# Kernel optimization log

Measured on AMD Instinct MI355X. Metric: run time of the kernel, lower is better.

Reference implementation:

```python
import jax, jax.numpy as jnp
import numpy as np

B, N = 32768, 20            # batch nodes, temporal neighbors
NF, EF, TF = 172, 172, 100  # node / edge / time feature dims
E = NF + TF                 # query_dim = 272
KD = NF + EF + TF           # key_dim = 444
H = 2                       # heads
HD = E // H                 # head dim 136
OUT = NF                    # output_dimension defaults to n_node_features
NEG = jnp.float32(-1e30)


def setup_inputs() -> dict:
    key = jax.random.key(0)
    ks = jax.random.split(key, 20)
    s = 0.02
    return {
        "src_node_features": jax.random.normal(ks[0], (B, NF), jnp.float32),
        "src_time_features": jax.random.normal(ks[1], (B, 1, TF), jnp.float32),
        "neighbor_features": jax.random.normal(ks[2], (B, N, NF), jnp.float32),
        "neighbor_time_features": jax.random.normal(ks[3], (B, N, TF), jnp.float32),
        "edge_features": jax.random.normal(ks[4], (B, N, EF), jnp.float32),
        "neighbor_mask": jax.random.bernoulli(ks[5], 0.3, (B, N)),
        # nn.MultiheadAttention params (separate q/k/v projections since kdim!=embed_dim)
        "q_w": jax.random.normal(ks[6], (E, E), jnp.float32) * s,
        "k_w": jax.random.normal(ks[7], (E, KD), jnp.float32) * s,
        "v_w": jax.random.normal(ks[8], (E, KD), jnp.float32) * s,
        "q_b": jnp.zeros((E,), jnp.float32),
        "k_b": jnp.zeros((E,), jnp.float32),
        "v_b": jnp.zeros((E,), jnp.float32),
        "out_w": jax.random.normal(ks[9], (E, E), jnp.float32) * s,
        "out_b": jnp.zeros((E,), jnp.float32),
        # merger MLP: Linear(E+NF -> OUT), ReLU, Linear(OUT -> OUT)
        "m1_w": jax.random.normal(ks[10], (OUT, E + NF), jnp.float32) * s,
        "m1_b": jnp.zeros((OUT,), jnp.float32),
        "m2_w": jax.random.normal(ks[11], (OUT, OUT), jnp.float32) * s,
        "m2_b": jnp.zeros((OUT,), jnp.float32),
    }


def reference(src_node_features, src_time_features, neighbor_features,
              neighbor_time_features, edge_features, neighbor_mask,
              q_w, k_w, v_w, q_b, k_b, v_b, out_w, out_b,
              m1_w, m1_b, m2_w, m2_b):
    b = src_node_features.shape[0]
    # single query per node: [B, E]
    query = jnp.concatenate([src_node_features, src_time_features[:, 0, :]], axis=1)
    # keys/values: [B, N, KD]
    kv = jnp.concatenate([neighbor_features, edge_features, neighbor_time_features], axis=2)

    # nodes with no valid neighbor: unmask position 0 (matches torch clone/set trick)
    invalid = jnp.all(neighbor_mask, axis=1)                      # [B]
    mask = neighbor_mask.at[:, 0].set(
        jnp.where(invalid, False, neighbor_mask[:, 0]))

    q = (query @ q_w.T + q_b).reshape(b, H, HD)                   # [B,H,HD]
    k = (kv @ k_w.T + k_b).reshape(b, N, H, HD)                   # [B,N,H,HD]
    v = (kv @ v_w.T + v_b).reshape(b, N, H, HD)

    scores = jnp.einsum('bhd,bnhd->bhn', q, k) / jnp.sqrt(jnp.float32(HD))
    scores = jnp.where(mask[:, None, :], NEG, scores)
    attn = jax.nn.softmax(scores, axis=-1)                        # [B,H,N]
    attn_weights = attn.mean(axis=1)                              # averaged over heads [B,N]

    ctx = jnp.einsum('bhn,bnhd->bhd', attn, v).reshape(b, E)
    attn_out = ctx @ out_w.T + out_b                              # [B,E]
    attn_out = jnp.where(invalid[:, None], 0.0, attn_out)

    merged = jnp.concatenate([attn_out, src_node_features], axis=1)
    hidden = jax.nn.relu(merged @ m1_w.T + m1_b)
    output = hidden @ m2_w.T + m2_b                               # [B,OUT]
    return output, attn_weights
```

## Files before the change

### kernel.cpp

```cpp
#include <hip/hip_runtime.h>
#include <hip/hip_bf16.h>
#include <math.h>

#define NF 172
#define TF_ 100
#define EF 172
#define EDIM 272
#define KD 444
#define NNB 20
#define HD 136
#define OUT_D 172

typedef __attribute__((ext_vector_type(4))) float f32x4;
typedef __attribute__((ext_vector_type(8))) __bf16 bf16x8;
typedef __attribute__((ext_vector_type(4))) __bf16 bf16x4;

__global__ void sniff_k(const unsigned char* __restrict__ m, int* __restrict__ flag) {
    __shared__ int c1, c2;
    if (threadIdx.x == 0) { c1 = 0; c2 = 0; }
    __syncthreads();
    for (int k = 0; k < 4; ++k) {
        int p = threadIdx.x * 4 + k;
        unsigned char v = m[p];
        if ((p & 3) != 0 && v)          atomicOr(&c1, 1);
        if ((p & 3) == 3 && v == 0x3f)  atomicOr(&c2, 1);
    }
    __syncthreads();
    if (threadIdx.x == 0) flag[0] = c2 ? 2 : (c1 ? 1 : 0);
}

#define BKP 40

__global__ __launch_bounds__(256) void gemm_mfma_k(
    const float* __restrict__ A0, int a0_cols, int a0_stride,
    const float* __restrict__ A1, int a1_stride,
    const float* __restrict__ W, int w_stride, int w_nn,
    const float* __restrict__ bias,
    const float* __restrict__ invalf,
    int relu,
    float* __restrict__ C, int c_stride,
    int N, int K)
{
    __shared__ __bf16 As[128][BKP];
    __shared__ __bf16 Bs[128][BKP];

    const int tid  = threadIdx.x;
    const int lane = tid & 63;
    const int wv   = tid >> 6;
    const int wr   = wv >> 1;
    const int wc   = wv & 1;
    const int lr   = lane & 15;
    const int lg   = lane >> 4;
    const int m0   = blockIdx.x * 128;
    const int n0   = blockIdx.y * 128;

    f32x4 acc[4][4];
#pragma unroll
    for (int i = 0; i < 4; ++i)
#pragma unroll
        for (int j = 0; j < 4; ++j) acc[i][j] = (f32x4)(0.f);

    const int srow = tid >> 1;
    const int sch0 = (tid & 1) * 4;
    const int tkk  = tid >> 3;
    const int tcb  = (tid & 7) * 16;

    const int ktiles = (K + 31) / 32;

    for (int t = 0; t < ktiles; ++t) {
        const int k0 = t * 32;

#pragma unroll
        for (int i = 0; i < 4; ++i) {
            const int ch = sch0 + i;
            const int k  = k0 + ch * 4;
            float4 v = make_float4(0.f, 0.f, 0.f, 0.f);
            if (k < K) {
                const float* p = (k < a0_cols)
                    ? (A0 + (size_t)(m0 + srow) * a0_stride + k)
                    : (A1 + (size_t)(m0 + srow) * a1_stride + (k - a0_cols));
                v = *(const float4*)p;
            }
            bf16x4 b;
            b[0] = (__bf16)v.x; b[1] = (__bf16)v.y;
            b[2] = (__bf16)v.z; b[3] = (__bf16)v.w;
            *(bf16x4*)&As[srow][ch * 4] = b;
        }

        if (!w_nn) {
#pragma unroll
            for (int i = 0; i < 4; ++i) {
                const int ch = sch0 + i;
                const int k  = k0 + ch * 4;
                float4 v = make_float4(0.f, 0.f, 0.f, 0.f);
                if (k < K && (n0 + srow) < N)
                    v = *(const float4*)(W + (size_t)(n0 + srow) * w_stride + k);
                bf16x4 b;
                b[0] = (__bf16)v.x; b[1] = (__bf16)v.y;
                b[2] = (__bf16)v.z; b[3] = (__bf16)v.w;
                *(bf16x4*)&Bs[srow][ch * 4] = b;
            }
        } else {
#pragma unroll
            for (int i = 0; i < 4; ++i) {
                const int c = tcb + i * 4;
                float4 v = make_float4(0.f, 0.f, 0.f, 0.f);
                if ((k0 + tkk) < K && (n0 + c + 3) < N)
                    v = *(const float4*)(W + (size_t)(k0 + tkk) * w_stride + n0 + c);
                Bs[c + 0][tkk] = (__bf16)v.x;
                Bs[c + 1][tkk] = (__bf16)v.y;
                Bs[c + 2][tkk] = (__bf16)v.z;
                Bs[c + 3][tkk] = (__bf16)v.w;
            }
        }
        __syncthreads();

        bf16x8 af[4], bfr[4];
#pragma unroll
        for (int f = 0; f < 4; ++f) {
            af[f]  = *(const bf16x8*)&As[wr * 64 + f * 16 + lr][lg * 8];
            bfr[f] = *(const bf16x8*)&Bs[wc * 64 + f * 16 + lr][lg * 8];
        }
#pragma unroll
        for (int fm = 0; fm < 4; ++fm)
#pragma unroll
            for (int fn = 0; fn < 4; ++fn)
                acc[fm][fn] = __builtin_amdgcn_mfma_f32_16x16x32_bf16(
                    af[fm], bfr[fn], acc[fm][fn], 0, 0, 0);
        __syncthreads();
    }

    float bv[4];
#pragma unroll
    for (int fn = 0; fn < 4; ++fn) {
        const int col = n0 + wc * 64 + fn * 16 + lr;
        bv[fn] = (bias && col < N) ? bias[col] : 0.f;
    }
#pragma unroll
    for (int fm = 0; fm < 4; ++fm) {
#pragma unroll
        for (int j = 0; j < 4; ++j) {
            const int row = m0 + wr * 64 + fm * 16 + lg * 4 + j;
            float zf = 1.f;
            if (invalf && invalf[row] != 0.f) zf = 0.f;
#pragma unroll
            for (int fn = 0; fn < 4; ++fn) {
                const int col = n0 + wc * 64 + fn * 16 + lr;
                if (col < N) {
                    float v = acc[fm][fn][j] + bv[fn];
                    if (relu) v = fmaxf(v, 0.f);
                    C[(size_t)row * c_stride + col] = v * zf;
                }
            }
        }
    }
}

__device__ __forceinline__ float dot4(float4 a, float4 b) {
    return a.x * b.x + a.y * b.y + a.z * b.z + a.w * b.w;
}

__global__ __launch_bounds__(256) void attn_flash_k(
    const float* __restrict__ nf, const float* __restrict__ ef,
    const float* __restrict__ ntf,
    const unsigned char* __restrict__ maskp,
    const int* __restrict__ mode_p,
    const float* __restrict__ qk,
    float* __restrict__ wkv,
    float* __restrict__ invalf,
    float* __restrict__ attnw)
{
    const int lane = threadIdx.x & 63;
    const int wv   = threadIdx.x >> 6;
    const int b    = blockIdx.x * 4 + wv;
    const int mode = mode_p[0];

    int mv = 0;
    if (lane < NNB) {
        if (mode == 0)      mv = ((const int*)maskp)[(size_t)b * NNB + lane] != 0;
        else if (mode == 1) mv = maskp[(size_t)b * NNB + lane] != 0;
        else                mv = ((const float*)maskp)[(size_t)b * NNB + lane] != 0.f;
    }
    unsigned long long bal = __ballot(lane < NNB && mv);
    const int inv = ((bal & 0xFFFFFULL) == 0xFFFFFULL);
    if (inv && lane == 0) mv = 0;
    if (lane == 0) invalf[b] = (float)inv;

    const float* qrow = qk + (size_t)b * 888;
    const float4 z4 = make_float4(0.f, 0.f, 0.f, 0.f);
    float4 q0a = *(const float4*)(qrow + lane * 4);
    float4 q1a = *(const float4*)(qrow + KD + lane * 4);
    float4 q0b = z4, q1b = z4;
    if (lane < 47) {
        q0b = *(const float4*)(qrow + (64 + lane) * 4);
        q1b = *(const float4*)(qrow + KD + (64 + lane) * 4);
    }

    const size_t rbase = (size_t)b * NNB;
    const float* pA;
    if (lane < 43) pA = nf + rbase * NF + lane * 4;
    else           pA = ef + rbase * EF + (lane - 43) * 4;
    const float* pB;
    int strideB;
    if (lane < 22) { pB = ef  + rbase * EF  + (21 + lane) * 4; strideB = EF;  }
    else           { pB = ntf + rbase * TF_ + (lane - 22) * 4; strideB = TF_; }

    const float scal = 0.08574929257125441f;
    float4 acc0a = z4, acc0b = z4, acc1a = z4, acc1b = z4;
    float m0 = -3.4e38f, m1 = -3.4e38f, s0 = 0.f, s1 = 0.f;
    float mys0 = 0.f, mys1 = 0.f;

#pragma unroll 5
    for (int n = 0; n < NNB; ++n) {
        float4 kA = *(const float4*)pA;
        pA += NF;
        float4 kB = z4;
        if (lane < 47) {
            kB = *(const float4*)pB;
            pB += strideB;
        }

        float p0 = dot4(q0a, kA) + dot4(q0b, kB);
        float p1 = dot4(q1a, kA) + dot4(q1b, kB);
#pragma unroll
        for (int off = 32; off; off >>= 1) {
            p0 += __shfl_xor(p0, off);
            p1 += __shfl_xor(p1, off);
        }

        const int mn = __shfl(mv, n);
        const float sc0 = mn ? -1e30f : p0 * scal;
        const float sc1 = mn ? -1e30f : p1 * scal;
        if (lane == n) { mys0 = sc0; mys1 = sc1; }

        {
            const float nm = fmaxf(m0, sc0);
            const float f  = expf(m0 - nm);
            const float p  = expf(sc0 - nm);
            s0 = s0 * f + p;
            acc0a.x = acc0a.x * f + p * kA.x;  acc0a.y = acc0a.y * f + p * kA.y;
            acc0a.z = acc0a.z * f + p * kA.z;  acc0a.w = acc0a.w * f + p * kA.w;
            acc0b.x = acc0b.x * f + p * kB.x;  acc0b.y = acc0b.y * f + p * kB.y;
            acc0b.z = acc0b.z * f + p * kB.z;  acc0b.w = acc0b.w * f + p * kB.w;
            m0 = nm;
        }
        {
            const float nm = fmaxf(m1, sc1);
            const float f  = expf(m1 - nm);
            const float p  = expf(sc1 - nm);
            s1 = s1 * f + p;
            acc1a.x = acc1a.x * f + p * kA.x;  acc1a.y = acc1a.y * f + p * kA.y;
            acc1a.z = acc1a.z * f + p * kA.z;  acc1a.w = acc1a.w * f + p * kA.w;
            acc1b.x = acc1b.x * f + p * kB.x;  acc1b.y = acc1b.y * f + p * kB.y;
            acc1b.z = acc1b.z * f + p * kB.z;  acc1b.w = acc1b.w * f + p * kB.w;
            m1 = nm;
        }
    }

    const float r0 = 1.f / s0;
    const float r1 = 1.f / s1;

    if (lane < NNB)
        attnw[(size_t)b * NNB + lane] =
            0.5f * (expf(mys0 - m0) * r0 + expf(mys1 - m1) * r1);

    float* wrow = wkv + (size_t)b * 888;
    float4 o;
    o.x = acc0a.x * r0; o.y = acc0a.y * r0; o.z = acc0a.z * r0; o.w = acc0a.w * r0;
    *(float4*)(wrow + lane * 4) = o;
    o.x = acc1a.x * r1; o.y = acc1a.y * r1; o.z = acc1a.z * r1; o.w = acc1a.w * r1;
    *(float4*)(wrow + KD + lane * 4) = o;
    if (lane < 47) {
        o.x = acc0b.x * r0; o.y = acc0b.y * r0; o.z = acc0b.z * r0; o.w = acc0b.w * r0;
        *(float4*)(wrow + (64 + lane) * 4) = o;
        o.x = acc1b.x * r1; o.y = acc1b.y * r1; o.z = acc1b.z * r1; o.w = acc1b.w * r1;
        *(float4*)(wrow + KD + (64 + lane) * 4) = o;
    }
}

extern "C" void kernel_launch(void* const* d_in, const int* in_sizes, int n_in,
                              void* d_out, int out_size, void* d_ws, size_t ws_size,
                              hipStream_t stream) {
    const float* src_node = (const float*)d_in[0];
    const float* src_time = (const float*)d_in[1];
    const float* nfp      = (const float*)d_in[2];
    const float* ntfp     = (const float*)d_in[3];
    const float* efp      = (const float*)d_in[4];
    const unsigned char* maskp = (const unsigned char*)d_in[5];
    const float* q_w   = (const float*)d_in[6];
    const float* k_w   = (const float*)d_in[7];
    const float* v_w   = (const float*)d_in[8];
    const float* q_b   = (const float*)d_in[9];
    const float* v_b   = (const float*)d_in[11];
    const float* out_w = (const float*)d_in[12];
    const float* out_b = (const float*)d_in[13];
    const float* m1_w  = (const float*)d_in[14];
    const float* m1_b  = (const float*)d_in[15];
    const float* m2_w  = (const float*)d_in[16];
    const float* m2_b  = (const float*)d_in[17];

    const int B = in_sizes[0] / NF;

    float* ws   = (float*)d_ws;
    int*   flag = (int*)d_ws;
    float* Qb   = ws + 16;
    float* qkb  = Qb + (size_t)B * 272;
    float* invb = qkb + (size_t)B * 888;
    float* aob  = qkb;
    float* hidb = Qb;
    float* outp  = (float*)d_out;
    float* attnw = outp + (size_t)B * OUT_D;

    const int gm = B / 128;

    sniff_k<<<1, 256, 0, stream>>>(maskp, flag);

    gemm_mfma_k<<<dim3(gm, 3), 256, 0, stream>>>(
        src_node, NF, NF, src_time, TF_,
        q_w, EDIM, 0, q_b, nullptr, 0, Qb, EDIM, EDIM, EDIM);

    for (int h = 0; h < 2; ++h) {
        gemm_mfma_k<<<dim3(gm, 4), 256, 0, stream>>>(
            Qb + h * HD, HD, EDIM, nullptr, 0,
            k_w + (size_t)h * HD * KD, KD, 1, nullptr, nullptr, 0,
            qkb + h * KD, 888, KD, HD);
    }

    attn_flash_k<<<B / 4, 256, 0, stream>>>(nfp, efp, ntfp, maskp, flag,
                                            qkb, qkb, invb, attnw);

    for (int h = 0; h < 2; ++h) {
        gemm_mfma_k<<<dim3(gm, 2), 256, 0, stream>>>(
            qkb + h * KD, KD, 888, nullptr, 0,
            v_w + (size_t)h * HD * KD, KD, 0, v_b + h * HD, nullptr, 0,
            Qb + h * HD, EDIM, HD, KD);
    }

    gemm_mfma_k<<<dim3(gm, 3), 256, 0, stream>>>(
        Qb, EDIM, EDIM, nullptr, 0,
        out_w, EDIM, 0, out_b, invb, 0, aob, EDIM, EDIM, EDIM);

    gemm_mfma_k<<<dim3(gm, 2), 256, 0, stream>>>(
        aob, EDIM, EDIM, src_node, NF,
        m1_w, KD, 0, m1_b, nullptr, 1, hidb, OUT_D, OUT_D, KD);

    gemm_mfma_k<<<dim3(gm, 2), 256, 0, stream>>>(
        hidb, OUT_D, OUT_D, nullptr, 0,
        m2_w, OUT_D, 0, m2_b, nullptr, 0, outp, OUT_D, OUT_D, OUT_D);
}
```

Measured before the change: 691.7 us.

## Fold Q·K and V·out weights into precomputed matrices, double-buffer GEMM, split attention

A prep kernel precomputes combined weights: q_w^T·k_w per head (GT, with a folded bias) and v_w^T·out_w (MT, with a folded bias). This replaces the Q GEMM, the two per-head QK GEMMs, the two V GEMMs and the out GEMM with one 272→888 GEMM and one 888→272 GEMM. The generic GEMM gains LDS double buffering with register prefetch and drops the transposed-weight path. The attention kernel splits each row's 20 neighbors across two waves, computes the softmax non-online through LDS, and merges partial accumulators. The weight folding is redone on every call, which adds a small prep kernel and enlarges the K dimension of the final GEMM.

```diff
diff --git a/kernel.cpp b/kernel.cpp
--- a/kernel.cpp
+++ b/kernel.cpp
@@ -29,20 +29,73 @@
     if (threadIdx.x == 0) flag[0] = c2 ? 2 : (c1 ? 1 : 0);
 }
 
+__global__ __launch_bounds__(256) void prep_k(
+    const float* __restrict__ q_w, const float* __restrict__ k_w,
+    const float* __restrict__ v_w, const float* __restrict__ q_b,
+    const float* __restrict__ v_b, const float* __restrict__ out_w,
+    const float* __restrict__ out_b,
+    float* __restrict__ GT, float* __restrict__ gb,
+    float* __restrict__ MT, float* __restrict__ mb)
+{
+    const int blk = blockIdx.x;
+    const int tid = threadIdx.x;
+    if (blk < 888) {
+        const int j = blk, h = j / 444, jj = j - h * 444;
+        for (int k = tid; k < 272; k += 256) {
+            float acc = 0.f;
+#pragma unroll 4
+            for (int c = 0; c < 136; ++c)
+                acc += q_w[(size_t)(h * 136 + c) * 272 + k] *
+                       k_w[(size_t)(h * 136 + c) * 444 + jj];
+            GT[(size_t)j * 272 + k] = acc;
+        }
+    } else if (blk < 888 + 272) {
+        const int j = blk - 888;
+        for (int r = tid; r < 888; r += 256) {
+            const int h = r / 444, d = r - h * 444;
+            float acc = 0.f;
+#pragma unroll 4
+            for (int c = 0; c < 136; ++c)
+                acc += v_w[(size_t)(h * 136 + c) * 444 + d] *
+                       out_w[(size_t)j * 272 + h * 136 + c];
+            MT[(size_t)j * 888 + r] = acc;
+        }
+    } else if (blk < 888 + 272 + 4) {
+        const int j = (blk - 888 - 272) * 256 + tid;
+        if (j < 888) {
+            const int h = j / 444, jj = j - h * 444;
+            float acc = 0.f;
+#pragma unroll 4
+            for (int c = 0; c < 136; ++c)
+                acc += q_b[h * 136 + c] * k_w[(size_t)(h * 136 + c) * 444 + jj];
+            gb[j] = acc;
+        }
+    } else {
+        const int j = (blk - 888 - 272 - 4) * 256 + tid;
+        if (j < 272) {
+            float acc = out_b[j];
+#pragma unroll 4
+            for (int e = 0; e < 272; ++e)
+                acc += v_b[e] * out_w[(size_t)j * 272 + e];
+            mb[j] = acc;
+        }
+    }
+}
+
 #define BKP 40
 
 __global__ __launch_bounds__(256) void gemm_mfma_k(
     const float* __restrict__ A0, int a0_cols, int a0_stride,
     const float* __restrict__ A1, int a1_stride,
-    const float* __restrict__ W, int w_stride, int w_nn,
+    const float* __restrict__ W, int w_stride,
     const float* __restrict__ bias,
     const float* __restrict__ invalf,
     int relu,
     float* __restrict__ C, int c_stride,
     int N, int K)
 {
-    __shared__ __bf16 As[128][BKP];
-    __shared__ __bf16 Bs[128][BKP];
+    __shared__ __bf16 As[2][128][BKP];
+    __shared__ __bf16 Bs[2][128][BKP];
 
     const int tid  = threadIdx.x;
     const int lane = tid & 63;
@@ -62,64 +115,51 @@
 
     const int srow = tid >> 1;
     const int sch0 = (tid & 1) * 4;
-    const int tkk  = tid >> 3;
-    const int tcb  = (tid & 7) * 16;
+    const float4 z4 = make_float4(0.f, 0.f, 0.f, 0.f);
+    float4 va[4], vb[4];
+
+#define LOAD_T(k0base) do {                                                   \
+    _Pragma("unroll")                                                         \
+    for (int i_ = 0; i_ < 4; ++i_) {                                          \
+        const int k_ = (k0base) + (sch0 + i_) * 4;                            \
+        va[i_] = z4; vb[i_] = z4;                                             \
+        if (k_ < K) {                                                         \
+            const float* p_ = (k_ < a0_cols)                                  \
+                ? (A0 + (size_t)(m0 + srow) * a0_stride + k_)                 \
+                : (A1 + (size_t)(m0 + srow) * a1_stride + (k_ - a0_cols));    \
+            va[i_] = *(const float4*)p_;                                      \
+            if ((n0 + srow) < N)                                              \
+                vb[i_] = *(const float4*)(W + (size_t)(n0 + srow) * w_stride + k_); \
+        }                                                                     \
+    } } while (0)
+
+#define STORE_T(bufi) do {                                                    \
+    _Pragma("unroll")                                                         \
+    for (int i_ = 0; i_ < 4; ++i_) {                                          \
+        bf16x4 ta_, tb_;                                                      \
+        ta_[0] = (__bf16)va[i_].x; ta_[1] = (__bf16)va[i_].y;                 \
+        ta_[2] = (__bf16)va[i_].z; ta_[3] = (__bf16)va[i_].w;                 \
+        tb_[0] = (__bf16)vb[i_].x; tb_[1] = (__bf16)vb[i_].y;                 \
+        tb_[2] = (__bf16)vb[i_].z; tb_[3] = (__bf16)vb[i_].w;                 \
+        *(bf16x4*)&As[bufi][srow][(sch0 + i_) * 4] = ta_;                     \
+        *(bf16x4*)&Bs[bufi][srow][(sch0 + i_) * 4] = tb_;                     \
+    } } while (0)
 
     const int ktiles = (K + 31) / 32;
-
+    LOAD_T(0);
+    STORE_T(0);
+    __syncthreads();
+
+    int cur = 0;
     for (int t = 0; t < ktiles; ++t) {
-        const int k0 = t * 32;
-
-#pragma unroll
-        for (int i = 0; i < 4; ++i) {
-            const int ch = sch0 + i;
-            const int k  = k0 + ch * 4;
-            float4 v = make_float4(0.f, 0.f, 0.f, 0.f);
-            if (k < K) {
-                const float* p = (k < a0_cols)
-                    ? (A0 + (size_t)(m0 + srow) * a0_stride + k)
-                    : (A1 + (size_t)(m0 + srow) * a1_stride + (k - a0_cols));
-                v = *(const float4*)p;
-            }
-            bf16x4 b;
-            b[0] = (__bf16)v.x; b[1] = (__bf16)v.y;
-            b[2] = (__bf16)v.z; b[3] = (__bf16)v.w;
-            *(bf16x4*)&As[srow][ch * 4] = b;
-        }
-
-        if (!w_nn) {
-#pragma unroll
-            for (int i = 0; i < 4; ++i) {
-                const int ch = sch0 + i;
-                const int k  = k0 + ch * 4;
-                float4 v = make_float4(0.f, 0.f, 0.f, 0.f);
-                if (k < K && (n0 + srow) < N)
-                    v = *(const float4*)(W + (size_t)(n0 + srow) * w_stride + k);
-                bf16x4 b;
-                b[0] = (__bf16)v.x; b[1] = (__bf16)v.y;
-                b[2] = (__bf16)v.z; b[3] = (__bf16)v.w;
-                *(bf16x4*)&Bs[srow][ch * 4] = b;
-            }
-        } else {
-#pragma unroll
-            for (int i = 0; i < 4; ++i) {
-                const int c = tcb + i * 4;
-                float4 v = make_float4(0.f, 0.f, 0.f, 0.f);
-                if ((k0 + tkk) < K && (n0 + c + 3) < N)
-                    v = *(const float4*)(W + (size_t)(k0 + tkk) * w_stride + n0 + c);
-                Bs[c + 0][tkk] = (__bf16)v.x;
-                Bs[c + 1][tkk] = (__bf16)v.y;
-                Bs[c + 2][tkk] = (__bf16)v.z;
-                Bs[c + 3][tkk] = (__bf16)v.w;
-            }
-        }
-        __syncthreads();
+        const int more = (t + 1 < ktiles);
+        if (more) LOAD_T((t + 1) * 32);
 
         bf16x8 af[4], bfr[4];
 #pragma unroll
         for (int f = 0; f < 4; ++f) {
-            af[f]  = *(const bf16x8*)&As[wr * 64 + f * 16 + lr][lg * 8];
-            bfr[f] = *(const bf16x8*)&Bs[wc * 64 + f * 16 + lr][lg * 8];
+            af[f]  = *(const bf16x8*)&As[cur][wr * 64 + f * 16 + lr][lg * 8];
+            bfr[f] = *(const bf16x8*)&Bs[cur][wc * 64 + f * 16 + lr][lg * 8];
         }
 #pragma unroll
         for (int fm = 0; fm < 4; ++fm)
@@ -127,8 +167,13 @@
             for (int fn = 0; fn < 4; ++fn)
                 acc[fm][fn] = __builtin_amdgcn_mfma_f32_16x16x32_bf16(
                     af[fm], bfr[fn], acc[fm][fn], 0, 0, 0);
+
+        if (more) STORE_T(cur ^ 1);
         __syncthreads();
-    }
+        cur ^= 1;
+    }
+#undef LOAD_T
+#undef STORE_T
 
     float bv[4];
 #pragma unroll
@@ -160,7 +205,7 @@
     return a.x * b.x + a.y * b.y + a.z * b.z + a.w * b.w;
 }
 
-__global__ __launch_bounds__(256) void attn_flash_k(
+__global__ __launch_bounds__(256) void attn_flash2_k(
     const float* __restrict__ nf, const float* __restrict__ ef,
     const float* __restrict__ ntf,
     const unsigned char* __restrict__ maskp,
@@ -170,9 +215,15 @@
     float* __restrict__ invalf,
     float* __restrict__ attnw)
 {
-    const int lane = threadIdx.x & 63;
-    const int wv   = threadIdx.x >> 6;
-    const int b    = blockIdx.x * 4 + wv;
+    __shared__ float  sc_lds[2][2][NNB];
+    __shared__ float4 acc_lds[2][4][64];
+
+    const int tid  = threadIdx.x;
+    const int lane = tid & 63;
+    const int wv   = tid >> 6;
+    const int rw   = wv >> 1;
+    const int hf   = wv & 1;
+    const int b    = blockIdx.x * 2 + rw;
     const int mode = mode_p[0];
 
     int mv = 0;
@@ -184,7 +235,7 @@
     unsigned long long bal = __ballot(lane < NNB && mv);
     const int inv = ((bal & 0xFFFFFULL) == 0xFFFFFULL);
     if (inv && lane == 0) mv = 0;
-    if (lane == 0) invalf[b] = (float)inv;
+    if (hf == 0 && lane == 0) invalf[b] = (float)inv;
 
     const float* qrow = qk + (size_t)b * 888;
     const float4 z4 = make_float4(0.f, 0.f, 0.f, 0.f);
@@ -196,7 +247,7 @@
         q1b = *(const float4*)(qrow + KD + (64 + lane) * 4);
     }
 
-    const size_t rbase = (size_t)b * NNB;
+    const size_t rbase = (size_t)b * NNB + hf * 10;
     const float* pA;
     if (lane < 43) pA = nf + rbase * NF + lane * 4;
     else           pA = ef + rbase * EF + (lane - 43) * 4;
@@ -205,76 +256,96 @@
     if (lane < 22) { pB = ef  + rbase * EF  + (21 + lane) * 4; strideB = EF;  }
     else           { pB = ntf + rbase * TF_ + (lane - 22) * 4; strideB = TF_; }
 
+    float4 kA[10], kB[10];
+#pragma unroll
+    for (int s = 0; s < 10; ++s) {
+        kA[s] = *(const float4*)pA; pA += NF;
+        kB[s] = z4;
+        if (lane < 47) { kB[s] = *(const float4*)pB; }
+        pB += strideB;
+    }
+
+    float s0v[10], s1v[10];
+#pragma unroll
+    for (int s = 0; s < 10; ++s) {
+        s0v[s] = dot4(q0a, kA[s]) + dot4(q0b, kB[s]);
+        s1v[s] = dot4(q1a, kA[s]) + dot4(q1b, kB[s]);
+    }
+#pragma unroll
+    for (int off = 32; off; off >>= 1) {
+#pragma unroll
+        for (int s = 0; s < 10; ++s) {
+            s0v[s] += __shfl_xor(s0v[s], off);
+            s1v[s] += __shfl_xor(s1v[s], off);
+        }
+    }
+
     const float scal = 0.08574929257125441f;
-    float4 acc0a = z4, acc0b = z4, acc1a = z4, acc1b = z4;
-    float m0 = -3.4e38f, m1 = -3.4e38f, s0 = 0.f, s1 = 0.f;
-    float mys0 = 0.f, mys1 = 0.f;
-
-#pragma unroll 5
-    for (int n = 0; n < NNB; ++n) {
-        float4 kA = *(const float4*)pA;
-        pA += NF;
-        float4 kB = z4;
+#pragma unroll
+    for (int s = 0; s < 10; ++s) {
+        const int g = hf * 10 + s;
+        const int mn = __shfl(mv, g);
+        s0v[s] = mn ? -1e30f : s0v[s] * scal;
+        s1v[s] = mn ? -1e30f : s1v[s] * scal;
+        if (lane == s) { sc_lds[rw][0][g] = s0v[s]; sc_lds[rw][1][g] = s1v[s]; }
+    }
+    __syncthreads();
+
+    float m0 = -3.4e38f, m1 = -3.4e38f;
+#pragma unroll
+    for (int g = 0; g < NNB; ++g) {
+        m0 = fmaxf(m0, sc_lds[rw][0][g]);
+        m1 = fmaxf(m1, sc_lds[rw][1][g]);
+    }
+    float sum0 = 0.f, sum1 = 0.f;
+#pragma unroll
+    for (int g = 0; g < NNB; ++g) {
+        sum0 += expf(sc_lds[rw][0][g] - m0);
+        sum1 += expf(sc_lds[rw][1][g] - m1);
+    }
+    const float r0 = 1.f / sum0;
+    const float r1 = 1.f / sum1;
+
+    float4 a0a = z4, a0b = z4, a1a = z4, a1b = z4;
+#pragma unroll
+    for (int s = 0; s < 10; ++s) {
+        const float w0 = expf(s0v[s] - m0) * r0;
+        const float w1 = expf(s1v[s] - m1) * r1;
+        a0a.x += w0 * kA[s].x; a0a.y += w0 * kA[s].y; a0a.z += w0 * kA[s].z; a0a.w += w0 * kA[s].w;
+        a0b.x += w0 * kB[s].x; a0b.y += w0 * kB[s].y; a0b.z += w0 * kB[s].z; a0b.w += w0 * kB[s].w;
+        a1a.x += w1 * kA[s].x; a1a.y += w1 * kA[s].y; a1a.z += w1 * kA[s].z; a1a.w += w1 * kA[s].w;
+        a1b.x += w1 * kB[s].x; a1b.y += w1 * kB[s].y; a1b.z += w1 * kB[s].z; a1b.w += w1 * kB[s].w;
+    }
+
+    if (hf == 1) {
+        acc_lds[rw][0][lane] = a0a;
+        acc_lds[rw][1][lane] = a0b;
+        acc_lds[rw][2][lane] = a1a;
+        acc_lds[rw][3][lane] = a1b;
+    }
+    __syncthreads();
+    if (hf == 0) {
+        float4 p0a = acc_lds[rw][0][lane], p0b = acc_lds[rw][1][lane];
+        float4 p1a = acc_lds[rw][2][lane], p1b = acc_lds[rw][3][lane];
+        a0a.x += p0a.x; a0a.y += p0a.y; a0a.z += p0a.z; a0a.w += p0a.w;
+        a0b.x += p0b.x; a0b.y += p0b.y; a0b.z += p0b.z; a0b.w += p0b.w;
+        a1a.x += p1a.x; a1a.y += p1a.y; a1a.z += p1a.z; a1a.w += p1a.w;
+        a1b.x += p1b.x; a1b.y += p1b.y; a1b.z += p1b.z; a1b.w += p1b.w;
+
+        float* wrow = wkv + (size_t)b * 888;
+        *(float4*)(wrow + lane * 4)      = a0a;
+        *(float4*)(wrow + KD + lane * 4) = a1a;
         if (lane < 47) {
-            kB = *(const float4*)pB;
-            pB += strideB;
-        }
-
-        float p0 = dot4(q0a, kA) + dot4(q0b, kB);
-        float p1 = dot4(q1a, kA) + dot4(q1b, kB);
-#pragma unroll
-        for (int off = 32; off; off >>= 1) {
-            p0 += __shfl_xor(p0, off);
-            p1 += __shfl_xor(p1, off);
-        }
-
-        const int mn = __shfl(mv, n);
-        const float sc0 = mn ? -1e30f : p0 * scal;
-        const float sc1 = mn ? -1e30f : p1 * scal;
-        if (lane == n) { mys0 = sc0; mys1 = sc1; }
-
-        {
-            const float nm = fmaxf(m0, sc0);
-            const float f  = expf(m0 - nm);
-            const float p  = expf(sc0 - nm);
-            s0 = s0 * f + p;
-            acc0a.x = acc0a.x * f + p * kA.x;  acc0a.y = acc0a.y * f + p * kA.y;
-            acc0a.z = acc0a.z * f + p * kA.z;  acc0a.w = acc0a.w * f + p * kA.w;
-            acc0b.x = acc0b.x * f + p * kB.x;  acc0b.y = acc0b.y * f + p * kB.y;
-            acc0b.z = acc0b.z * f + p * kB.z;  acc0b.w = acc0b.w * f + p * kB.w;
-            m0 = nm;
-        }
-        {
-            const float nm = fmaxf(m1, sc1);
-            const float f  = expf(m1 - nm);
-            const float p  = expf(sc1 - nm);
-            s1 = s1 * f + p;
-            acc1a.x = acc1a.x * f + p * kA.x;  acc1a.y = acc1a.y * f + p * kA.y;
-            acc1a.z = acc1a.z * f + p * kA.z;  acc1a.w = acc1a.w * f + p * kA.w;
-            acc1b.x = acc1b.x * f + p * kB.x;  acc1b.y = acc1b.y * f + p * kB.y;
-            acc1b.z = acc1b.z * f + p * kB.z;  acc1b.w = acc1b.w * f + p * kB.w;
-            m1 = nm;
-        }
-    }
-
-    const float r0 = 1.f / s0;
-    const float r1 = 1.f / s1;
-
-    if (lane < NNB)
-        attnw[(size_t)b * NNB + lane] =
-            0.5f * (expf(mys0 - m0) * r0 + expf(mys1 - m1) * r1);
-
-    float* wrow = wkv + (size_t)b * 888;
-    float4 o;
-    o.x = acc0a.x * r0; o.y = acc0a.y * r0; o.z = acc0a.z * r0; o.w = acc0a.w * r0;
-    *(float4*)(wrow + lane * 4) = o;
-    o.x = acc1a.x * r1; o.y = acc1a.y * r1; o.z = acc1a.z * r1; o.w = acc1a.w * r1;
-    *(float4*)(wrow + KD + lane * 4) = o;
-    if (lane < 47) {
-        o.x = acc0b.x * r0; o.y = acc0b.y * r0; o.z = acc0b.z * r0; o.w = acc0b.w * r0;
-        *(float4*)(wrow + (64 + lane) * 4) = o;
-        o.x = acc1b.x * r1; o.y = acc1b.y * r1; o.z = acc1b.z * r1; o.w = acc1b.w * r1;
-        *(float4*)(wrow + KD + (64 + lane) * 4) = o;
+            *(float4*)(wrow + (64 + lane) * 4)      = a0b;
+            *(float4*)(wrow + KD + (64 + lane) * 4) = a1b;
+        }
+#pragma unroll
+        for (int g = 0; g < NNB; ++g) {
+            if (lane == g)
+                attnw[(size_t)b * NNB + g] =
+                    0.5f * (expf(sc_lds[rw][0][g] - m0) * r0 +
+                            expf(sc_lds[rw][1][g] - m1) * r1);
+        }
     }
 }
 
@@ -303,48 +374,39 @@
 
     float* ws   = (float*)d_ws;
     int*   flag = (int*)d_ws;
-    float* Qb   = ws + 16;
-    float* qkb  = Qb + (size_t)B * 272;
+    float* qkb  = ws + 16;
     float* invb = qkb + (size_t)B * 888;
-    float* aob  = qkb;
-    float* hidb = Qb;
+    float* aob  = invb + B;
+    float* GT   = aob + (size_t)B * 272;
+    float* gb   = GT + 888 * 272;
+    float* MT   = gb + 888;
+    float* mb   = MT + 272 * 888;
+    float* hidb = qkb;
     float* outp  = (float*)d_out;
     float* attnw = outp + (size_t)B * OUT_D;
 
     const int gm = B / 128;
 
     sniff_k<<<1, 256, 0, stream>>>(maskp, flag);
+    prep_k<<<1166, 256, 0, stream>>>(q_w, k_w, v_w, q_b, v_b, out_w, out_b,
+                                     GT, gb, MT, mb);
+
+    gemm_mfma_k<<<dim3(gm, 7), 256, 0, stream>>>(
+        src_node, NF, NF, src_time, TF_,
+        GT, 272, gb, nullptr, 0, qkb, 888, 888, 272);
+
+    attn_flash2_k<<<B / 2, 256, 0, stream>>>(nfp, efp, ntfp, maskp, flag,
+                                             qkb, qkb, invb, attnw);
 
     gemm_mfma_k<<<dim3(gm, 3), 256, 0, stream>>>(
-        src_node, NF, NF, src_time, TF_,
-        q_w, EDIM, 0, q_b, nullptr, 0, Qb, EDIM, EDIM, EDIM);
-
-    for (int h = 0; h < 2; ++h) {
-        gemm_mfma_k<<<dim3(gm, 4), 256, 0, stream>>>(
-            Qb + h * HD, HD, EDIM, nullptr, 0,
-            k_w + (size_t)h * HD * KD, KD, 1, nullptr, nullptr, 0,
-            qkb + h * KD, 888, KD, HD);
-    }
-
-    attn_flash_k<<<B / 4, 256, 0, stream>>>(nfp, efp, ntfp, maskp, flag,
-                                            qkb, qkb, invb, attnw);
-
-    for (int h = 0; h < 2; ++h) {
-        gemm_mfma_k<<<dim3(gm, 2), 256, 0, stream>>>(
-            qkb + h * KD, KD, 888, nullptr, 0,
-            v_w + (size_t)h * HD * KD, KD, 0, v_b + h * HD, nullptr, 0,
-            Qb + h * HD, EDIM, HD, KD);
-    }
-
-    gemm_mfma_k<<<dim3(gm, 3), 256, 0, stream>>>(
-        Qb, EDIM, EDIM, nullptr, 0,
-        out_w, EDIM, 0, out_b, invb, 0, aob, EDIM, EDIM, EDIM);
+        qkb, 888, 888, nullptr, 0,
+        MT, 888, mb, invb, 0, aob, 272, 272, 888);
 
     gemm_mfma_k<<<dim3(gm, 2), 256, 0, stream>>>(
         aob, EDIM, EDIM, src_node, NF,
-        m1_w, KD, 0, m1_b, nullptr, 1, hidb, OUT_D, OUT_D, KD);
+        m1_w, KD, m1_b, nullptr, 1, hidb, OUT_D, OUT_D, KD);
 
     gemm_mfma_k<<<dim3(gm, 2), 256, 0, stream>>>(
         hidb, OUT_D, OUT_D, nullptr, 0,
-        m2_w, OUT_D, 0, m2_b, nullptr, 0, outp, OUT_D, OUT_D, OUT_D);
-}
+        m2_w, OUT_D, m2_b, nullptr, 0, outp, OUT_D, OUT_D, OUT_D);
+}
```

New measurement: 718.3 us. 1.04x slower.
